# Optimization experiments

Measured on AMD Instinct MI355X. Metric: run time of the kernel, lower is better.

The kernel has to match this reference:

```python
import jax, jax.numpy as jnp
import numpy as np

MUL = 32           # multiplicity of each irrep (0e and 1e) in inputs and output
E = 50000          # number of edges
DIM = 4 * MUL      # 32x0e (32) + 32x1e (96) = 128

# e3nn FullyConnectedTensorProduct normalization (irrep_normalization='component',
# path_normalization='element'):
#   output 0e: paths (0e,0e->0e),(1e,1e->0e): alpha = dim(0e)/ (1024+1024) -> sqrt(1/2048)
#   output 1e: paths (0e,1e),(1e,0e),(1e,1e): alpha = dim(1e)/(3*1024)    -> sqrt(1/1024)
C_OUT0 = (1.0 / 2048.0) ** 0.5
C_OUT1 = (1.0 / 1024.0) ** 0.5
# real-basis Wigner 3j constants (e3nn conventions):
#   w3j(1,1,0) = delta_ij/sqrt(3); w3j(0,1,1)=w3j(1,0,1)=delta/sqrt(3); w3j(1,1,1)=eps_ijk/sqrt(6)
INV_SQRT3 = 3.0 ** -0.5
INV_SQRT6 = 6.0 ** -0.5


def _levi_civita():
    e = np.zeros((3, 3, 3), dtype=np.float32)
    e[0, 1, 2] = e[1, 2, 0] = e[2, 0, 1] = 1.0
    e[0, 2, 1] = e[2, 1, 0] = e[1, 0, 2] = -1.0
    return jnp.asarray(e)


def setup_inputs() -> dict:
    key = jax.random.key(0)
    ks = jax.random.split(key, 7)
    wshape = (MUL, MUL, MUL)  # uvw weights per path (e3nn init: standard normal)
    return {
        "x1": jax.random.normal(ks[0], (E, DIM), dtype=jnp.float32),
        "x2": jax.random.normal(ks[1], (E, DIM), dtype=jnp.float32),
        "W000": jax.random.normal(ks[2], wshape, dtype=jnp.float32),
        "W110": jax.random.normal(ks[3], wshape, dtype=jnp.float32),
        "W011": jax.random.normal(ks[4], wshape, dtype=jnp.float32),
        "W101": jax.random.normal(ks[5], wshape, dtype=jnp.float32),
        "W111": jax.random.normal(ks[6], wshape, dtype=jnp.float32),
    }


def reference(x1, x2, W000, W110, W011, W101, W111):
    # split irreps: [E, 32] scalars (0e), [E, 32, 3] vectors (1e), mul-major layout
    a0, a1 = x1[:, :MUL], x1[:, MUL:].reshape(-1, MUL, 3)
    b0, b1 = x2[:, :MUL], x2[:, MUL:].reshape(-1, MUL, 3)
    eps = _levi_civita()

    # scalar (0e) output: 0e x 0e -> 0e  and  1e . 1e -> 0e
    out0 = C_OUT0 * (
        jnp.einsum('uvw,eu,ev->ew', W000, a0, b0)
        + INV_SQRT3 * jnp.einsum('uvw,eui,evi->ew', W110, a1, b1)
    )

    # vector (1e) output: 0e*1e -> 1e, 1e*0e -> 1e, 1e x 1e -> 1e (cross product)
    out1 = C_OUT1 * (
        INV_SQRT3 * (
            jnp.einsum('uvw,eu,evk->ewk', W011, a0, b1)
            + jnp.einsum('uvw,euk,ev->ewk', W101, a1, b0)
        )
        + INV_SQRT6 * jnp.einsum('uvw,ijk,eui,evj->ewk', W111, eps, a1, b1)
    )

    return jnp.concatenate([out0, out1.reshape(-1, MUL * 3)], axis=1)  # [E, 128]
```

## Files before the change

### kernel.cpp

```cpp
#include <hip/hip_runtime.h>
#include <hip/hip_bf16.h>


typedef __attribute__((ext_vector_type(8))) short short8;
typedef __attribute__((ext_vector_type(4))) float f32x4;

static constexpr float C_OUT0    = 0.022097086912079608f;
static constexpr float C_OUT1    = 0.03125f;
static constexpr float INV_SQRT3 = 0.57735026918962576f;
static constexpr float INV_SQRT6 = 0.40824829046386302f;

static __device__ __forceinline__ short bfbits(float x) {
    __hip_bfloat16 h = __float2bfloat16(x);
    return __builtin_bit_cast(short, h);
}

__global__ __launch_bounds__(256) void prep_weights(
    const float* __restrict__ W000, const float* __restrict__ W110,
    const float* __restrict__ W011, const float* __restrict__ W101,
    const float* __restrict__ W111, short* __restrict__ wsB)
{
    const int t = blockIdx.x * 256 + threadIdx.x;
    if (t >= 5 * 32768) return;
    const int g   = t >> 15;
    const int idx = t & 32767;
    const int u = idx >> 10, v = (idx >> 5) & 31, w = idx & 31;
    const float* Wp = (g == 0) ? W000 : (g == 1) ? W110 : (g == 2) ? W011
                    : (g == 3) ? W101 : W111;
    const float s = (g == 0) ? C_OUT0
                  : (g == 1) ? C_OUT0 * INV_SQRT3
                  : (g == 4) ? C_OUT1 * INV_SQRT6
                  :            C_OUT1 * INV_SQRT3;
    const int f = 2 * g + (w >> 4);
    const int l = ((u >> 3) << 4) | (w & 15);
    const int j = u & 7;
    wsB[(((v * 10 + f) * 64) + l) * 8 + j] = bfbits(s * Wp[idx]);
}

__global__ __launch_bounds__(256) void e3nn_vsplit(
    const float* __restrict__ x1, const float* __restrict__ x2,
    const short8* __restrict__ wsB, float* __restrict__ out, int E)
{
    __shared__ float smemf[32 * 132];
    float4* smem4 = (float4*)smemf;

    const int tid   = threadIdx.x;
    const int l     = tid & 63;
    const int wv    = tid >> 6;
    const int t     = wv & 1;
    const int vh    = wv >> 1;
    const int eBase = blockIdx.x * 32;

    const float4* x1v = (const float4*)x1;
    for (int i = tid; i < 32 * 32; i += 256) {
        const int e = i >> 5, c4 = i & 31;
        float4 val = {0.f, 0.f, 0.f, 0.f};
        if (eBase + e < E) val = x1v[(size_t)(eBase + e) * 32 + c4];
        smem4[e * 33 + c4] = val;
    }
    __syncthreads();

    const int eloc = l & 15;
    const int u0   = (l >> 4) * 8;
    const float* row = smemf + (t * 16 + eloc) * 132;
    float a0r[8], a1r[3][8];
    #pragma unroll
    for (int j = 0; j < 8; ++j) {
        a0r[j] = row[u0 + j];
        #pragma unroll
        for (int c = 0; c < 3; ++c)
            a1r[c][j] = row[32 + 3 * (u0 + j) + c];
    }
    __syncthreads();

    for (int i = tid; i < 32 * 128; i += 256) {
        const int e = i >> 7, r = i & 127;
        float val = 0.f;
        if (eBase + e < E) val = x2[(size_t)(eBase + e) * 128 + r];
        if (r < 32) {
            smemf[e * 132 + r * 4] = val;
        } else {
            const int q = r - 32, vv = q / 3, c = q - 3 * vv;
            smemf[e * 132 + vv * 4 + 1 + c] = val;
        }
    }
    __syncthreads();

    const f32x4 zero = {0.f, 0.f, 0.f, 0.f};
    f32x4 acc0[2]    = {zero, zero};
    f32x4 acc1[3][2] = {{zero, zero}, {zero, zero}, {zero, zero}};

    const short8* wb    = wsB + l;
    const float4* bsrow = smem4 + (t * 16 + eloc) * 33;

    for (int v = vh * 16; v < vh * 16 + 16; ++v) {
        const float4 b = bsrow[v];
        const short8* p = wb + v * 640;
        short8 Bf[10];
        #pragma unroll
        for (int i = 0; i < 10; ++i) Bf[i] = p[i * 64];

        const float bv[3] = {b.y, b.z, b.w};
        short8 A;

        #pragma unroll
        for (int j = 0; j < 8; ++j) A[j] = bfbits(a0r[j] * b.x);
        acc0[0] = __builtin_amdgcn_mfma_f32_16x16x32_bf16(A, Bf[0], acc0[0], 0, 0, 0);
        acc0[1] = __builtin_amdgcn_mfma_f32_16x16x32_bf16(A, Bf[1], acc0[1], 0, 0, 0);

        #pragma unroll
        for (int j = 0; j < 8; ++j)
            A[j] = bfbits(a1r[0][j] * b.y + a1r[1][j] * b.z + a1r[2][j] * b.w);
        acc0[0] = __builtin_amdgcn_mfma_f32_16x16x32_bf16(A, Bf[2], acc0[0], 0, 0, 0);
        acc0[1] = __builtin_amdgcn_mfma_f32_16x16x32_bf16(A, Bf[3], acc0[1], 0, 0, 0);

        #pragma unroll
        for (int kx = 0; kx < 3; ++kx) {
            const int ii = (kx + 1) % 3, jj = (kx + 2) % 3;
            short8 A011, A101, A111;
            #pragma unroll
            for (int j = 0; j < 8; ++j) {
                A011[j] = bfbits(a0r[j] * bv[kx]);
                A101[j] = bfbits(a1r[kx][j] * b.x);
                A111[j] = bfbits(a1r[ii][j] * bv[jj] - a1r[jj][j] * bv[ii]);
            }
            acc1[kx][0] = __builtin_amdgcn_mfma_f32_16x16x32_bf16(A011, Bf[4], acc1[kx][0], 0, 0, 0);
            acc1[kx][1] = __builtin_amdgcn_mfma_f32_16x16x32_bf16(A011, Bf[5], acc1[kx][1], 0, 0, 0);
            acc1[kx][0] = __builtin_amdgcn_mfma_f32_16x16x32_bf16(A101, Bf[6], acc1[kx][0], 0, 0, 0);
            acc1[kx][1] = __builtin_amdgcn_mfma_f32_16x16x32_bf16(A101, Bf[7], acc1[kx][1], 0, 0, 0);
            acc1[kx][0] = __builtin_amdgcn_mfma_f32_16x16x32_bf16(A111, Bf[8], acc1[kx][0], 0, 0, 0);
            acc1[kx][1] = __builtin_amdgcn_mfma_f32_16x16x32_bf16(A111, Bf[9], acc1[kx][1], 0, 0, 0);
        }
    }

    __syncthreads();

    float* red = smemf;
    const int rbase = (t * 64 + l) * 33;
    if (vh == 1) {
        #pragma unroll
        for (int nf = 0; nf < 2; ++nf)
            #pragma unroll
            for (int r = 0; r < 4; ++r) {
                red[rbase + (0 + nf) * 4 + r] = acc0[nf][r];
                red[rbase + (2 + nf) * 4 + r] = acc1[0][nf][r];
                red[rbase + (4 + nf) * 4 + r] = acc1[1][nf][r];
                red[rbase + (6 + nf) * 4 + r] = acc1[2][nf][r];
            }
    }
    __syncthreads();

    if (vh == 0) {
        const int be0 = t * 16 + (l >> 4) * 4;
        #pragma unroll
        for (int nf = 0; nf < 2; ++nf) {
            const int w = nf * 16 + (l & 15);
            #pragma unroll
            for (int r = 0; r < 4; ++r) {
                const int ge = eBase + be0 + r;
                if (ge < E) {
                    const size_t base = (size_t)ge * 128;
                    out[base + w] =
                        acc0[nf][r] + red[rbase + (0 + nf) * 4 + r];
                    out[base + 32 + 3 * w + 0] =
                        acc1[0][nf][r] + red[rbase + (2 + nf) * 4 + r];
                    out[base + 32 + 3 * w + 1] =
                        acc1[1][nf][r] + red[rbase + (4 + nf) * 4 + r];
                    out[base + 32 + 3 * w + 2] =
                        acc1[2][nf][r] + red[rbase + (6 + nf) * 4 + r];
                }
            }
        }
    }
}

extern "C" void kernel_launch(void* const* d_in, const int* in_sizes, int n_in,
                              void* d_out, int out_size, void* d_ws, size_t ws_size,
                              hipStream_t stream) {
    const float* x1   = (const float*)d_in[0];
    const float* x2   = (const float*)d_in[1];
    const float* W000 = (const float*)d_in[2];
    const float* W110 = (const float*)d_in[3];
    const float* W011 = (const float*)d_in[4];
    const float* W101 = (const float*)d_in[5];
    const float* W111 = (const float*)d_in[6];
    float* out = (float*)d_out;

    const int E = in_sizes[0] / 128;

    hipLaunchKernelGGL(prep_weights, dim3((5 * 32768 + 255) / 256), dim3(256), 0, stream,
                       W000, W110, W011, W101, W111, (short*)d_ws);

    const int grid = (E + 31) / 32;
    hipLaunchKernelGGL(e3nn_vsplit, dim3(grid), dim3(256), 0, stream,
                       x1, x2, (const short8*)d_ws, out, E);
}
```

Measured before the change: 83.99 us.

## Stage weight fragments through double-buffered LDS and drop the v-split reduction

Each block now handles 64 edges with each of the four waves owning 16 edges over all 32 v values, so the cross-wave shared-memory reduction is gone. The per-v weight fragments are streamed into LDS with global_load_lds using a double buffer, prefetching the next v while MFMAs run on the current one. x2 is stored in LDS as bf16 in a v-major layout. The cost is a __syncthreads per v iteration, longer serial MFMA chains per wave, and extra bf16 rounding of x2 before the products.

Measured after the change: 109.4 us. 30.2% more time.

```diff
diff --git a/kernel.cpp b/kernel.cpp
--- a/kernel.cpp
+++ b/kernel.cpp
@@ -4,6 +4,10 @@
 
 typedef __attribute__((ext_vector_type(8))) short short8;
 typedef __attribute__((ext_vector_type(4))) float f32x4;
+typedef __attribute__((ext_vector_type(4))) unsigned short u16x4;
+
+#define AS_GLOBAL __attribute__((address_space(1)))
+#define AS_LOCAL  __attribute__((address_space(3)))
 
 static constexpr float C_OUT0    = 0.022097086912079608f;
 static constexpr float C_OUT1    = 0.03125f;
@@ -13,6 +17,14 @@
 static __device__ __forceinline__ short bfbits(float x) {
     __hip_bfloat16 h = __float2bfloat16(x);
     return __builtin_bit_cast(short, h);
+}
+static __device__ __forceinline__ float b2f(unsigned short u) {
+    unsigned int x = ((unsigned int)u) << 16;
+    return __builtin_bit_cast(float, x);
+}
+static __device__ __forceinline__ void gload_lds16(const void* g, void* l) {
+    __builtin_amdgcn_global_load_lds((const AS_GLOBAL unsigned int*)g,
+                                     (AS_LOCAL unsigned int*)l, 16, 0, 0);
 }
 
 __global__ __launch_bounds__(256) void prep_weights(
@@ -37,32 +49,32 @@
     wsB[(((v * 10 + f) * 64) + l) * 8 + j] = bfbits(s * Wp[idx]);
 }
 
-__global__ __launch_bounds__(256) void e3nn_vsplit(
+__global__ __launch_bounds__(256, 4) void e3nn_stage(
     const float* __restrict__ x1, const float* __restrict__ x2,
     const short8* __restrict__ wsB, float* __restrict__ out, int E)
 {
-    __shared__ float smemf[32 * 132];
-    float4* smem4 = (float4*)smemf;
+    __shared__ __align__(16) char smem[36864];
+    float4*         x1s = (float4*)smem;
+    unsigned short* bsu = (unsigned short*)smem;
+    char*          ldsB = smem + 16384;
 
     const int tid   = threadIdx.x;
     const int l     = tid & 63;
     const int wv    = tid >> 6;
-    const int t     = wv & 1;
-    const int vh    = wv >> 1;
-    const int eBase = blockIdx.x * 32;
+    const int eBase = blockIdx.x * 64;
 
     const float4* x1v = (const float4*)x1;
-    for (int i = tid; i < 32 * 32; i += 256) {
+    for (int i = tid; i < 64 * 32; i += 256) {
         const int e = i >> 5, c4 = i & 31;
         float4 val = {0.f, 0.f, 0.f, 0.f};
         if (eBase + e < E) val = x1v[(size_t)(eBase + e) * 32 + c4];
-        smem4[e * 33 + c4] = val;
+        x1s[e * 33 + c4] = val;
     }
     __syncthreads();
 
     const int eloc = l & 15;
     const int u0   = (l >> 4) * 8;
-    const float* row = smemf + (t * 16 + eloc) * 132;
+    const float* row = (const float*)(x1s + ((wv * 16 + eloc) * 33));
     float a0r[8], a1r[3][8];
     #pragma unroll
     for (int j = 0; j < 8; ++j) {
@@ -73,15 +85,25 @@
     }
     __syncthreads();
 
-    for (int i = tid; i < 32 * 128; i += 256) {
+    for (int i = tid; i < 64 * 128; i += 256) {
         const int e = i >> 7, r = i & 127;
         float val = 0.f;
         if (eBase + e < E) val = x2[(size_t)(eBase + e) * 128 + r];
+        const unsigned short hb = (unsigned short)bfbits(val);
         if (r < 32) {
-            smemf[e * 132 + r * 4] = val;
+            bsu[(r * 64 + e) * 4 + 0] = hb;
         } else {
             const int q = r - 32, vv = q / 3, c = q - 3 * vv;
-            smemf[e * 132 + vv * 4 + 1 + c] = val;
+            bsu[(vv * 64 + e) * 4 + 1 + c] = hb;
+        }
+    }
+    {
+        const char* g = (const char*)wsB;
+        #pragma unroll
+        for (int r = 0; r < 3; ++r) {
+            const int chunk = r * 256 + wv * 64;
+            if (chunk < 640)
+                gload_lds16(g + (chunk + l) * 16, ldsB + chunk * 16);
         }
     }
     __syncthreads();
@@ -90,30 +112,38 @@
     f32x4 acc0[2]    = {zero, zero};
     f32x4 acc1[3][2] = {{zero, zero}, {zero, zero}, {zero, zero}};
 
-    const short8* wb    = wsB + l;
-    const float4* bsrow = smem4 + (t * 16 + eloc) * 33;
-
-    for (int v = vh * 16; v < vh * 16 + 16; ++v) {
-        const float4 b = bsrow[v];
-        const short8* p = wb + v * 640;
-        short8 Bf[10];
-        #pragma unroll
-        for (int i = 0; i < 10; ++i) Bf[i] = p[i * 64];
-
-        const float bv[3] = {b.y, b.z, b.w};
+    const unsigned short* bsrow = bsu + (wv * 16 + eloc) * 4;
+
+    for (int v = 0; v < 32; ++v) {
+        const int cur = v & 1;
+        if (v + 1 < 32) {
+            const char* g  = (const char*)wsB + (v + 1) * 10240;
+            char*       lb = ldsB + (cur ^ 1) * 10240;
+            #pragma unroll
+            for (int r = 0; r < 3; ++r) {
+                const int chunk = r * 256 + wv * 64;
+                if (chunk < 640)
+                    gload_lds16(g + (chunk + l) * 16, lb + chunk * 16);
+            }
+        }
+
+        const u16x4 bq = *(const u16x4*)(bsrow + v * 256);
+        const float b0 = b2f(bq.x), bx = b2f(bq.y), by = b2f(bq.z), bz = b2f(bq.w);
+        const float bv[3] = {bx, by, bz};
+
+        const char* bb = ldsB + cur * 10240;
+        #define BFRAG(f) (*(const short8*)(bb + (((f) * 64) + l) * 16))
+
         short8 A;
-
-        #pragma unroll
-        for (int j = 0; j < 8; ++j) A[j] = bfbits(a0r[j] * b.x);
-        acc0[0] = __builtin_amdgcn_mfma_f32_16x16x32_bf16(A, Bf[0], acc0[0], 0, 0, 0);
-        acc0[1] = __builtin_amdgcn_mfma_f32_16x16x32_bf16(A, Bf[1], acc0[1], 0, 0, 0);
-
+        #pragma unroll
+        for (int j = 0; j < 8; ++j) A[j] = bfbits(a0r[j] * b0);
+        acc0[0] = __builtin_amdgcn_mfma_f32_16x16x32_bf16(A, BFRAG(0), acc0[0], 0, 0, 0);
+        acc0[1] = __builtin_amdgcn_mfma_f32_16x16x32_bf16(A, BFRAG(1), acc0[1], 0, 0, 0);
         #pragma unroll
         for (int j = 0; j < 8; ++j)
-            A[j] = bfbits(a1r[0][j] * b.y + a1r[1][j] * b.z + a1r[2][j] * b.w);
-        acc0[0] = __builtin_amdgcn_mfma_f32_16x16x32_bf16(A, Bf[2], acc0[0], 0, 0, 0);
-        acc0[1] = __builtin_amdgcn_mfma_f32_16x16x32_bf16(A, Bf[3], acc0[1], 0, 0, 0);
-
+            A[j] = bfbits(a1r[0][j] * bx + a1r[1][j] * by + a1r[2][j] * bz);
+        acc0[0] = __builtin_amdgcn_mfma_f32_16x16x32_bf16(A, BFRAG(2), acc0[0], 0, 0, 0);
+        acc0[1] = __builtin_amdgcn_mfma_f32_16x16x32_bf16(A, BFRAG(3), acc0[1], 0, 0, 0);
         #pragma unroll
         for (int kx = 0; kx < 3; ++kx) {
             const int ii = (kx + 1) % 3, jj = (kx + 2) % 3;
@@ -121,54 +151,34 @@
             #pragma unroll
             for (int j = 0; j < 8; ++j) {
                 A011[j] = bfbits(a0r[j] * bv[kx]);
-                A101[j] = bfbits(a1r[kx][j] * b.x);
+                A101[j] = bfbits(a1r[kx][j] * b0);
                 A111[j] = bfbits(a1r[ii][j] * bv[jj] - a1r[jj][j] * bv[ii]);
             }
-            acc1[kx][0] = __builtin_amdgcn_mfma_f32_16x16x32_bf16(A011, Bf[4], acc1[kx][0], 0, 0, 0);
-            acc1[kx][1] = __builtin_amdgcn_mfma_f32_16x16x32_bf16(A011, Bf[5], acc1[kx][1], 0, 0, 0);
-            acc1[kx][0] = __builtin_amdgcn_mfma_f32_16x16x32_bf16(A101, Bf[6], acc1[kx][0], 0, 0, 0);
-            acc1[kx][1] = __builtin_amdgcn_mfma_f32_16x16x32_bf16(A101, Bf[7], acc1[kx][1], 0, 0, 0);
-            acc1[kx][0] = __builtin_amdgcn_mfma_f32_16x16x32_bf16(A111, Bf[8], acc1[kx][0], 0, 0, 0);
-            acc1[kx][1] = __builtin_amdgcn_mfma_f32_16x16x32_bf16(A111, Bf[9], acc1[kx][1], 0, 0, 0);
-        }
-    }
-
-    __syncthreads();
-
-    float* red = smemf;
-    const int rbase = (t * 64 + l) * 33;
-    if (vh == 1) {
-        #pragma unroll
-        for (int nf = 0; nf < 2; ++nf)
-            #pragma unroll
-            for (int r = 0; r < 4; ++r) {
-                red[rbase + (0 + nf) * 4 + r] = acc0[nf][r];
-                red[rbase + (2 + nf) * 4 + r] = acc1[0][nf][r];
-                red[rbase + (4 + nf) * 4 + r] = acc1[1][nf][r];
-                red[rbase + (6 + nf) * 4 + r] = acc1[2][nf][r];
-            }
-    }
-    __syncthreads();
-
-    if (vh == 0) {
-        const int be0 = t * 16 + (l >> 4) * 4;
-        #pragma unroll
-        for (int nf = 0; nf < 2; ++nf) {
-            const int w = nf * 16 + (l & 15);
-            #pragma unroll
-            for (int r = 0; r < 4; ++r) {
-                const int ge = eBase + be0 + r;
-                if (ge < E) {
-                    const size_t base = (size_t)ge * 128;
-                    out[base + w] =
-                        acc0[nf][r] + red[rbase + (0 + nf) * 4 + r];
-                    out[base + 32 + 3 * w + 0] =
-                        acc1[0][nf][r] + red[rbase + (2 + nf) * 4 + r];
-                    out[base + 32 + 3 * w + 1] =
-                        acc1[1][nf][r] + red[rbase + (4 + nf) * 4 + r];
-                    out[base + 32 + 3 * w + 2] =
-                        acc1[2][nf][r] + red[rbase + (6 + nf) * 4 + r];
-                }
+            acc1[kx][0] = __builtin_amdgcn_mfma_f32_16x16x32_bf16(A011, BFRAG(4), acc1[kx][0], 0, 0, 0);
+            acc1[kx][1] = __builtin_amdgcn_mfma_f32_16x16x32_bf16(A011, BFRAG(5), acc1[kx][1], 0, 0, 0);
+            acc1[kx][0] = __builtin_amdgcn_mfma_f32_16x16x32_bf16(A101, BFRAG(6), acc1[kx][0], 0, 0, 0);
+            acc1[kx][1] = __builtin_amdgcn_mfma_f32_16x16x32_bf16(A101, BFRAG(7), acc1[kx][1], 0, 0, 0);
+            acc1[kx][0] = __builtin_amdgcn_mfma_f32_16x16x32_bf16(A111, BFRAG(8), acc1[kx][0], 0, 0, 0);
+            acc1[kx][1] = __builtin_amdgcn_mfma_f32_16x16x32_bf16(A111, BFRAG(9), acc1[kx][1], 0, 0, 0);
+        }
+        #undef BFRAG
+
+        __syncthreads();
+    }
+
+    const int be0 = wv * 16 + (l >> 4) * 4;
+    #pragma unroll
+    for (int nf = 0; nf < 2; ++nf) {
+        const int w = nf * 16 + (l & 15);
+        #pragma unroll
+        for (int r = 0; r < 4; ++r) {
+            const int ge = eBase + be0 + r;
+            if (ge < E) {
+                const size_t base = (size_t)ge * 128;
+                out[base + w]              = acc0[nf][r];
+                out[base + 32 + 3 * w + 0] = acc1[0][nf][r];
+                out[base + 32 + 3 * w + 1] = acc1[1][nf][r];
+                out[base + 32 + 3 * w + 2] = acc1[2][nf][r];
             }
         }
     }
@@ -191,7 +201,7 @@
     hipLaunchKernelGGL(prep_weights, dim3((5 * 32768 + 255) / 256), dim3(256), 0, stream,
                        W000, W110, W011, W101, W111, (short*)d_ws);
 
-    const int grid = (E + 31) / 32;
-    hipLaunchKernelGGL(e3nn_vsplit, dim3(grid), dim3(256), 0, stream,
+    const int grid = (E + 63) / 64;
+    hipLaunchKernelGGL(e3nn_stage, dim3(grid), dim3(256), 0, stream,
                        x1, x2, (const short8*)d_ws, out, E);
 }
```

## Switch to 32x32x16 MFMA tiles with 64 edges per block

Applied to the files above, without the earlier changes.

Replaces the 16x16x32 bf16 MFMA scheme with 32x32x16 MFMAs. Each wave now covers 32 edges by 32 outputs and splits the u dimension into two halves, with the weight prep layout reshuffled to match. Each block processes 64 edges instead of 32, so the weight fragments loaded per v step are reused across twice as many edges, which cuts weight traffic relative to compute. In exchange it uses more LDS and accumulator registers, which may lower occupancy, and there are half as many blocks.

Result: slower. 130.3 us (+55.1%).

```diff
diff --git a/kernel.cpp b/kernel.cpp
--- a/kernel.cpp
+++ b/kernel.cpp
@@ -2,8 +2,8 @@
 #include <hip/hip_bf16.h>
 
 
-typedef __attribute__((ext_vector_type(8))) short short8;
-typedef __attribute__((ext_vector_type(4))) float f32x4;
+typedef __attribute__((ext_vector_type(8)))  short short8;
+typedef __attribute__((ext_vector_type(16))) float f32x16;
 
 static constexpr float C_OUT0    = 0.022097086912079608f;
 static constexpr float C_OUT1    = 0.03125f;
@@ -31,28 +31,29 @@
                   : (g == 1) ? C_OUT0 * INV_SQRT3
                   : (g == 4) ? C_OUT1 * INV_SQRT6
                   :            C_OUT1 * INV_SQRT3;
-    const int f = 2 * g + (w >> 4);
-    const int l = ((u >> 3) << 4) | (w & 15);
+    const int h = (u >> 4) & 1;
+    const int f = 2 * g + h;
+    const int l = (((u >> 3) & 1) << 5) | w;
     const int j = u & 7;
     wsB[(((v * 10 + f) * 64) + l) * 8 + j] = bfbits(s * Wp[idx]);
 }
 
-__global__ __launch_bounds__(256) void e3nn_vsplit(
+__global__ __launch_bounds__(256) void e3nn_m32(
     const float* __restrict__ x1, const float* __restrict__ x2,
     const short8* __restrict__ wsB, float* __restrict__ out, int E)
 {
-    __shared__ float smemf[32 * 132];
+    __shared__ __align__(16) float smemf[64 * 132];
     float4* smem4 = (float4*)smemf;
 
     const int tid   = threadIdx.x;
     const int l     = tid & 63;
     const int wv    = tid >> 6;
-    const int t     = wv & 1;
+    const int tile  = wv & 1;
     const int vh    = wv >> 1;
-    const int eBase = blockIdx.x * 32;
+    const int eBase = blockIdx.x * 64;
 
     const float4* x1v = (const float4*)x1;
-    for (int i = tid; i < 32 * 32; i += 256) {
+    for (int i = tid; i < 64 * 32; i += 256) {
         const int e = i >> 5, c4 = i & 31;
         float4 val = {0.f, 0.f, 0.f, 0.f};
         if (eBase + e < E) val = x1v[(size_t)(eBase + e) * 32 + c4];
@@ -60,20 +61,23 @@
     }
     __syncthreads();
 
-    const int eloc = l & 15;
-    const int u0   = (l >> 4) * 8;
-    const float* row = smemf + (t * 16 + eloc) * 132;
-    float a0r[8], a1r[3][8];
+    const int erow = l & 31;
+    const int kg   = l >> 5;
+    const float* row = smemf + (tile * 32 + erow) * 132;
+    float a0r[2][8], a1r[3][2][8];
     #pragma unroll
-    for (int j = 0; j < 8; ++j) {
-        a0r[j] = row[u0 + j];
+    for (int h = 0; h < 2; ++h)
         #pragma unroll
-        for (int c = 0; c < 3; ++c)
-            a1r[c][j] = row[32 + 3 * (u0 + j) + c];
-    }
+        for (int j = 0; j < 8; ++j) {
+            const int u = 16 * h + 8 * kg + j;
+            a0r[h][j]    = row[u];
+            a1r[0][h][j] = row[32 + 3 * u + 0];
+            a1r[1][h][j] = row[32 + 3 * u + 1];
+            a1r[2][h][j] = row[32 + 3 * u + 2];
+        }
     __syncthreads();
 
-    for (int i = tid; i < 32 * 128; i += 256) {
+    for (int i = tid; i < 64 * 128; i += 256) {
         const int e = i >> 7, r = i & 127;
         float val = 0.f;
         if (eBase + e < E) val = x2[(size_t)(eBase + e) * 128 + r];
@@ -86,89 +90,78 @@
     }
     __syncthreads();
 
-    const f32x4 zero = {0.f, 0.f, 0.f, 0.f};
-    f32x4 acc0[2]    = {zero, zero};
-    f32x4 acc1[3][2] = {{zero, zero}, {zero, zero}, {zero, zero}};
+    const f32x16 zero16 = {0.f,0.f,0.f,0.f,0.f,0.f,0.f,0.f,
+                           0.f,0.f,0.f,0.f,0.f,0.f,0.f,0.f};
+    f32x16 acc0    = zero16;
+    f32x16 acc1[3] = {zero16, zero16, zero16};
 
     const short8* wb    = wsB + l;
-    const float4* bsrow = smem4 + (t * 16 + eloc) * 33;
+    const float4* bsrow = smem4 + (tile * 32 + erow) * 33;
 
-    for (int v = vh * 16; v < vh * 16 + 16; ++v) {
+    for (int i = 0; i < 16; ++i) {
+        const int v = vh * 16 + i;
         const float4 b = bsrow[v];
         const short8* p = wb + v * 640;
         short8 Bf[10];
         #pragma unroll
-        for (int i = 0; i < 10; ++i) Bf[i] = p[i * 64];
+        for (int f = 0; f < 10; ++f) Bf[f] = p[f * 64];
 
         const float bv[3] = {b.y, b.z, b.w};
-        short8 A;
 
         #pragma unroll
-        for (int j = 0; j < 8; ++j) A[j] = bfbits(a0r[j] * b.x);
-        acc0[0] = __builtin_amdgcn_mfma_f32_16x16x32_bf16(A, Bf[0], acc0[0], 0, 0, 0);
-        acc0[1] = __builtin_amdgcn_mfma_f32_16x16x32_bf16(A, Bf[1], acc0[1], 0, 0, 0);
-
-        #pragma unroll
-        for (int j = 0; j < 8; ++j)
-            A[j] = bfbits(a1r[0][j] * b.y + a1r[1][j] * b.z + a1r[2][j] * b.w);
-        acc0[0] = __builtin_amdgcn_mfma_f32_16x16x32_bf16(A, Bf[2], acc0[0], 0, 0, 0);
-        acc0[1] = __builtin_amdgcn_mfma_f32_16x16x32_bf16(A, Bf[3], acc0[1], 0, 0, 0);
-
-        #pragma unroll
-        for (int kx = 0; kx < 3; ++kx) {
-            const int ii = (kx + 1) % 3, jj = (kx + 2) % 3;
-            short8 A011, A101, A111;
+        for (int h = 0; h < 2; ++h) {
+            short8 A;
             #pragma unroll
-            for (int j = 0; j < 8; ++j) {
-                A011[j] = bfbits(a0r[j] * bv[kx]);
-                A101[j] = bfbits(a1r[kx][j] * b.x);
-                A111[j] = bfbits(a1r[ii][j] * bv[jj] - a1r[jj][j] * bv[ii]);
+            for (int j = 0; j < 8; ++j) A[j] = bfbits(a0r[h][j] * b.x);
+            acc0 = __builtin_amdgcn_mfma_f32_32x32x16_bf16(A, Bf[0 + h], acc0, 0, 0, 0);
+            #pragma unroll
+            for (int j = 0; j < 8; ++j)
+                A[j] = bfbits(a1r[0][h][j] * b.y + a1r[1][h][j] * b.z + a1r[2][h][j] * b.w);
+            acc0 = __builtin_amdgcn_mfma_f32_32x32x16_bf16(A, Bf[2 + h], acc0, 0, 0, 0);
+            #pragma unroll
+            for (int kx = 0; kx < 3; ++kx) {
+                const int ii = (kx + 1) % 3, jj = (kx + 2) % 3;
+                short8 A011, A101, A111;
+                #pragma unroll
+                for (int j = 0; j < 8; ++j) {
+                    A011[j] = bfbits(a0r[h][j] * bv[kx]);
+                    A101[j] = bfbits(a1r[kx][h][j] * b.x);
+                    A111[j] = bfbits(a1r[ii][h][j] * bv[jj] - a1r[jj][h][j] * bv[ii]);
+                }
+                acc1[kx] = __builtin_amdgcn_mfma_f32_32x32x16_bf16(A011, Bf[4 + h], acc1[kx], 0, 0, 0);
+                acc1[kx] = __builtin_amdgcn_mfma_f32_32x32x16_bf16(A101, Bf[6 + h], acc1[kx], 0, 0, 0);
+                acc1[kx] = __builtin_amdgcn_mfma_f32_32x32x16_bf16(A111, Bf[8 + h], acc1[kx], 0, 0, 0);
             }
-            acc1[kx][0] = __builtin_amdgcn_mfma_f32_16x16x32_bf16(A011, Bf[4], acc1[kx][0], 0, 0, 0);
-            acc1[kx][1] = __builtin_amdgcn_mfma_f32_16x16x32_bf16(A011, Bf[5], acc1[kx][1], 0, 0, 0);
-            acc1[kx][0] = __builtin_amdgcn_mfma_f32_16x16x32_bf16(A101, Bf[6], acc1[kx][0], 0, 0, 0);
-            acc1[kx][1] = __builtin_amdgcn_mfma_f32_16x16x32_bf16(A101, Bf[7], acc1[kx][1], 0, 0, 0);
-            acc1[kx][0] = __builtin_amdgcn_mfma_f32_16x16x32_bf16(A111, Bf[8], acc1[kx][0], 0, 0, 0);
-            acc1[kx][1] = __builtin_amdgcn_mfma_f32_16x16x32_bf16(A111, Bf[9], acc1[kx][1], 0, 0, 0);
         }
     }
 
     __syncthreads();
 
     float* red = smemf;
-    const int rbase = (t * 64 + l) * 33;
+    const int w = erow;
     if (vh == 1) {
         #pragma unroll
-        for (int nf = 0; nf < 2; ++nf)
-            #pragma unroll
-            for (int r = 0; r < 4; ++r) {
-                red[rbase + (0 + nf) * 4 + r] = acc0[nf][r];
-                red[rbase + (2 + nf) * 4 + r] = acc1[0][nf][r];
-                red[rbase + (4 + nf) * 4 + r] = acc1[1][nf][r];
-                red[rbase + (6 + nf) * 4 + r] = acc1[2][nf][r];
-            }
+        for (int r = 0; r < 16; ++r) {
+            const int eloc = tile * 32 + (r & 3) + 8 * (r >> 2) + 4 * kg;
+            red[eloc * 132 + 0 * 33 + w] = acc0[r];
+            red[eloc * 132 + 1 * 33 + w] = acc1[0][r];
+            red[eloc * 132 + 2 * 33 + w] = acc1[1][r];
+            red[eloc * 132 + 3 * 33 + w] = acc1[2][r];
+        }
     }
     __syncthreads();
 
     if (vh == 0) {
-        const int be0 = t * 16 + (l >> 4) * 4;
         #pragma unroll
-        for (int nf = 0; nf < 2; ++nf) {
-            const int w = nf * 16 + (l & 15);
-            #pragma unroll
-            for (int r = 0; r < 4; ++r) {
-                const int ge = eBase + be0 + r;
-                if (ge < E) {
-                    const size_t base = (size_t)ge * 128;
-                    out[base + w] =
-                        acc0[nf][r] + red[rbase + (0 + nf) * 4 + r];
-                    out[base + 32 + 3 * w + 0] =
-                        acc1[0][nf][r] + red[rbase + (2 + nf) * 4 + r];
-                    out[base + 32 + 3 * w + 1] =
-                        acc1[1][nf][r] + red[rbase + (4 + nf) * 4 + r];
-                    out[base + 32 + 3 * w + 2] =
-                        acc1[2][nf][r] + red[rbase + (6 + nf) * 4 + r];
-                }
+        for (int r = 0; r < 16; ++r) {
+            const int eloc = tile * 32 + (r & 3) + 8 * (r >> 2) + 4 * kg;
+            const int ge = eBase + eloc;
+            if (ge < E) {
+                const size_t base = (size_t)ge * 128;
+                out[base + w]              = acc0[r]    + red[eloc * 132 + 0 * 33 + w];
+                out[base + 32 + 3 * w + 0] = acc1[0][r] + red[eloc * 132 + 1 * 33 + w];
+                out[base + 32 + 3 * w + 1] = acc1[1][r] + red[eloc * 132 + 2 * 33 + w];
+                out[base + 32 + 3 * w + 2] = acc1[2][r] + red[eloc * 132 + 3 * 33 + w];
             }
         }
     }
@@ -191,7 +184,7 @@
     hipLaunchKernelGGL(prep_weights, dim3((5 * 32768 + 255) / 256), dim3(256), 0, stream,
                        W000, W110, W011, W101, W111, (short*)d_ws);
 
-    const int grid = (E + 31) / 32;
-    hipLaunchKernelGGL(e3nn_vsplit, dim3(grid), dim3(256), 0, stream,
+    const int grid = (E + 63) / 64;
+    hipLaunchKernelGGL(e3nn_m32, dim3(grid), dim3(256), 0, stream,
                        x1, x2, (const short8*)d_ws, out, E);
 }
```

## Factor x2 scaling out of MFMA operands, apply it to fp32 MFMA outputs

Applied to the files above, without the earlier changes.

Restructures the per-v inner loop so the MFMA A operands come only from x1 (converted to bf16 once). The x2 coefficients are then applied with fp32 vector multiply-adds on the MFMA results, including the cross-product terms. This removes most per-iteration bf16 conversions and product building on the VALU. In exchange it issues slightly more MFMAs per step, adds a shared-memory transpose of x2 with vectorised loads, and roughly doubles LDS use.

Result: faster. 81.27 us (-3.2%).

```diff
diff --git a/kernel.cpp b/kernel.cpp
--- a/kernel.cpp
+++ b/kernel.cpp
@@ -37,12 +37,13 @@
     wsB[(((v * 10 + f) * 64) + l) * 8 + j] = bfbits(s * Wp[idx]);
 }
 
-__global__ __launch_bounds__(256) void e3nn_vsplit(
+__global__ __launch_bounds__(256) void e3nn_ts(
     const float* __restrict__ x1, const float* __restrict__ x2,
     const short8* __restrict__ wsB, float* __restrict__ out, int E)
 {
-    __shared__ float smemf[32 * 132];
-    float4* smem4 = (float4*)smemf;
+    __shared__ __align__(16) float rawS[32 * 132];
+    __shared__ __align__(16) float bT[128 * 36];
+    float4* raw4 = (float4*)rawS;
 
     const int tid   = threadIdx.x;
     const int l     = tid & 63;
@@ -56,32 +57,46 @@
         const int e = i >> 5, c4 = i & 31;
         float4 val = {0.f, 0.f, 0.f, 0.f};
         if (eBase + e < E) val = x1v[(size_t)(eBase + e) * 32 + c4];
-        smem4[e * 33 + c4] = val;
+        raw4[e * 33 + c4] = val;
     }
     __syncthreads();
 
     const int eloc = l & 15;
     const int u0   = (l >> 4) * 8;
-    const float* row = smemf + (t * 16 + eloc) * 132;
-    float a0r[8], a1r[3][8];
-    #pragma unroll
-    for (int j = 0; j < 8; ++j) {
-        a0r[j] = row[u0 + j];
-        #pragma unroll
-        for (int c = 0; c < 3; ++c)
-            a1r[c][j] = row[32 + 3 * (u0 + j) + c];
-    }
-    __syncthreads();
-
-    for (int i = tid; i < 32 * 128; i += 256) {
-        const int e = i >> 7, r = i & 127;
-        float val = 0.f;
-        if (eBase + e < E) val = x2[(size_t)(eBase + e) * 128 + r];
-        if (r < 32) {
-            smemf[e * 132 + r * 4] = val;
-        } else {
-            const int q = r - 32, vv = q / 3, c = q - 3 * vv;
-            smemf[e * 132 + vv * 4 + 1 + c] = val;
+    {
+        const float* row = rawS + (t * 16 + eloc) * 132;
+    }
+    short8 Aa0, Aax, Aay, Aaz;
+    {
+        const float* row = rawS + (t * 16 + eloc) * 132;
+        #pragma unroll
+        for (int j = 0; j < 8; ++j) {
+            Aa0[j] = bfbits(row[u0 + j]);
+            Aax[j] = bfbits(row[32 + 3 * (u0 + j) + 0]);
+            Aay[j] = bfbits(row[32 + 3 * (u0 + j) + 1]);
+            Aaz[j] = bfbits(row[32 + 3 * (u0 + j) + 2]);
+        }
+    }
+    __syncthreads();
+
+    const float4* x2v = (const float4*)x2;
+    for (int i = tid; i < 32 * 32; i += 256) {
+        const int e = i >> 5, c4 = i & 31;
+        float4 val = {0.f, 0.f, 0.f, 0.f};
+        if (eBase + e < E) val = x2v[(size_t)(eBase + e) * 32 + c4];
+        raw4[e * 33 + c4] = val;
+    }
+    __syncthreads();
+
+    {
+        const int s  = tid >> 1;
+        const int eh = tid & 1;
+        const int v  = s >> 2, c = s & 3;
+        const int r  = (c == 0) ? v : (32 + v * 3 + (c - 1));
+        #pragma unroll
+        for (int ee = 0; ee < 16; ++ee) {
+            const int e = eh * 16 + ee;
+            bT[s * 36 + e] = rawS[e * 132 + r];
         }
     }
     __syncthreads();
@@ -90,52 +105,53 @@
     f32x4 acc0[2]    = {zero, zero};
     f32x4 acc1[3][2] = {{zero, zero}, {zero, zero}, {zero, zero}};
 
-    const short8* wb    = wsB + l;
-    const float4* bsrow = smem4 + (t * 16 + eloc) * 33;
-
+    const short8* wb  = wsB + l;
+    const float*  bTt = bT + t * 16 + (l >> 4) * 4;
+
+    #pragma unroll 2
     for (int v = vh * 16; v < vh * 16 + 16; ++v) {
-        const float4 b = bsrow[v];
         const short8* p = wb + v * 640;
         short8 Bf[10];
         #pragma unroll
-        for (int i = 0; i < 10; ++i) Bf[i] = p[i * 64];
-
-        const float bv[3] = {b.y, b.z, b.w};
-        short8 A;
-
-        #pragma unroll
-        for (int j = 0; j < 8; ++j) A[j] = bfbits(a0r[j] * b.x);
-        acc0[0] = __builtin_amdgcn_mfma_f32_16x16x32_bf16(A, Bf[0], acc0[0], 0, 0, 0);
-        acc0[1] = __builtin_amdgcn_mfma_f32_16x16x32_bf16(A, Bf[1], acc0[1], 0, 0, 0);
-
-        #pragma unroll
-        for (int j = 0; j < 8; ++j)
-            A[j] = bfbits(a1r[0][j] * b.y + a1r[1][j] * b.z + a1r[2][j] * b.w);
-        acc0[0] = __builtin_amdgcn_mfma_f32_16x16x32_bf16(A, Bf[2], acc0[0], 0, 0, 0);
-        acc0[1] = __builtin_amdgcn_mfma_f32_16x16x32_bf16(A, Bf[3], acc0[1], 0, 0, 0);
-
-        #pragma unroll
-        for (int kx = 0; kx < 3; ++kx) {
-            const int ii = (kx + 1) % 3, jj = (kx + 2) % 3;
-            short8 A011, A101, A111;
-            #pragma unroll
-            for (int j = 0; j < 8; ++j) {
-                A011[j] = bfbits(a0r[j] * bv[kx]);
-                A101[j] = bfbits(a1r[kx][j] * b.x);
-                A111[j] = bfbits(a1r[ii][j] * bv[jj] - a1r[jj][j] * bv[ii]);
-            }
-            acc1[kx][0] = __builtin_amdgcn_mfma_f32_16x16x32_bf16(A011, Bf[4], acc1[kx][0], 0, 0, 0);
-            acc1[kx][1] = __builtin_amdgcn_mfma_f32_16x16x32_bf16(A011, Bf[5], acc1[kx][1], 0, 0, 0);
-            acc1[kx][0] = __builtin_amdgcn_mfma_f32_16x16x32_bf16(A101, Bf[6], acc1[kx][0], 0, 0, 0);
-            acc1[kx][1] = __builtin_amdgcn_mfma_f32_16x16x32_bf16(A101, Bf[7], acc1[kx][1], 0, 0, 0);
-            acc1[kx][0] = __builtin_amdgcn_mfma_f32_16x16x32_bf16(A111, Bf[8], acc1[kx][0], 0, 0, 0);
-            acc1[kx][1] = __builtin_amdgcn_mfma_f32_16x16x32_bf16(A111, Bf[9], acc1[kx][1], 0, 0, 0);
-        }
-    }
-
-    __syncthreads();
-
-    float* red = smemf;
+        for (int f = 0; f < 10; ++f) Bf[f] = p[f * 64];
+
+        const f32x4 B0 = *(const f32x4*)(bTt + (v * 4 + 0) * 36);
+        const f32x4 Bx = *(const f32x4*)(bTt + (v * 4 + 1) * 36);
+        const f32x4 By = *(const f32x4*)(bTt + (v * 4 + 2) * 36);
+        const f32x4 Bz = *(const f32x4*)(bTt + (v * 4 + 3) * 36);
+
+        #pragma unroll
+        for (int nf = 0; nf < 2; ++nf) {
+            const f32x4 G000  = __builtin_amdgcn_mfma_f32_16x16x32_bf16(Aa0, Bf[0 + nf], zero, 0, 0, 0);
+            const f32x4 G110x = __builtin_amdgcn_mfma_f32_16x16x32_bf16(Aax, Bf[2 + nf], zero, 0, 0, 0);
+            const f32x4 G110y = __builtin_amdgcn_mfma_f32_16x16x32_bf16(Aay, Bf[2 + nf], zero, 0, 0, 0);
+            const f32x4 G110z = __builtin_amdgcn_mfma_f32_16x16x32_bf16(Aaz, Bf[2 + nf], zero, 0, 0, 0);
+            acc0[nf] += B0 * G000 + Bx * G110x + By * G110y + Bz * G110z;
+
+            const f32x4 G011  = __builtin_amdgcn_mfma_f32_16x16x32_bf16(Aa0, Bf[4 + nf], zero, 0, 0, 0);
+            acc1[0][nf] += Bx * G011;
+            acc1[1][nf] += By * G011;
+            acc1[2][nf] += Bz * G011;
+
+            const f32x4 G101x = __builtin_amdgcn_mfma_f32_16x16x32_bf16(Aax, Bf[6 + nf], zero, 0, 0, 0);
+            const f32x4 G101y = __builtin_amdgcn_mfma_f32_16x16x32_bf16(Aay, Bf[6 + nf], zero, 0, 0, 0);
+            const f32x4 G101z = __builtin_amdgcn_mfma_f32_16x16x32_bf16(Aaz, Bf[6 + nf], zero, 0, 0, 0);
+            acc1[0][nf] += B0 * G101x;
+            acc1[1][nf] += B0 * G101y;
+            acc1[2][nf] += B0 * G101z;
+
+            const f32x4 G111x = __builtin_amdgcn_mfma_f32_16x16x32_bf16(Aax, Bf[8 + nf], zero, 0, 0, 0);
+            const f32x4 G111y = __builtin_amdgcn_mfma_f32_16x16x32_bf16(Aay, Bf[8 + nf], zero, 0, 0, 0);
+            const f32x4 G111z = __builtin_amdgcn_mfma_f32_16x16x32_bf16(Aaz, Bf[8 + nf], zero, 0, 0, 0);
+            acc1[0][nf] += Bz * G111y - By * G111z;
+            acc1[1][nf] += Bx * G111z - Bz * G111x;
+            acc1[2][nf] += By * G111x - Bx * G111y;
+        }
+    }
+
+    __syncthreads();
+
+    float* red = rawS;
     const int rbase = (t * 64 + l) * 33;
     if (vh == 1) {
         #pragma unroll
@@ -192,6 +208,6 @@
                        W000, W110, W011, W101, W111, (short*)d_ws);
 
     const int grid = (E + 31) / 32;
-    hipLaunchKernelGGL(e3nn_vsplit, dim3(grid), dim3(256), 0, stream,
+    hipLaunchKernelGGL(e3nn_ts, dim3(grid), dim3(256), 0, stream,
                        x1, x2, (const short8*)d_ws, out, E);
 }
```
